# Performance work log

Hardware: AMD Instinct MI355X
Metric: run time of the kernel (lower is better)

Reference implementation:

```python
import jax, jax.numpy as jnp
import numpy as np

N_NODES = 50000
N_EDGES = 800000
NFEAT, NHID, NCLASS = 256, 128, 47


def _gcn_norm(edge_index, edge_weight, n):
    """PyG GCNConv normalization: add self-loops (weight 1) then symmetric deg^-1/2."""
    src, dst = edge_index[0], edge_index[1]
    loop = jnp.arange(n, dtype=src.dtype)
    src_f = jnp.concatenate([src, loop])
    dst_f = jnp.concatenate([dst, loop])
    w_f = jnp.concatenate([edge_weight, jnp.ones((n,), edge_weight.dtype)])
    deg = jax.ops.segment_sum(w_f, dst_f, num_segments=n)  # [n]
    deg_safe = jnp.where(deg > 0, deg, 1.0)
    dinv = jnp.where(deg > 0, jax.lax.rsqrt(deg_safe), 0.0)
    norm = dinv[src_f] * w_f * dinv[dst_f]  # [E + n]
    return src_f, dst_f, norm


def _gcn_conv(h, src, dst, norm, b, n):
    # gather transformed source features, scale, scatter-add into targets
    msg = h[src] * norm[:, None]  # [E+n, d]
    return jax.ops.segment_sum(msg, dst, num_segments=n) + b


def setup_inputs() -> dict:
    key = jax.random.key(0)
    k = jax.random.split(key, 8)
    x = jax.random.normal(k[0], (N_NODES, NFEAT), dtype=jnp.float32)
    edge_index = jax.random.randint(k[1], (2, N_EDGES), 0, N_NODES, dtype=jnp.int32)
    edge_weight = jax.random.uniform(k[2], (N_EDGES,), dtype=jnp.float32)
    W1 = jax.random.normal(k[3], (NFEAT, NHID), dtype=jnp.float32) * (1.0 / np.sqrt(NFEAT))
    b1 = jnp.zeros((NHID,), dtype=jnp.float32)
    W2 = jax.random.normal(k[4], (NHID, NCLASS), dtype=jnp.float32) * (1.0 / np.sqrt(NHID))
    b2 = jnp.zeros((NCLASS,), dtype=jnp.float32)
    return {"x": x, "edge_index": edge_index, "edge_weight": edge_weight,
            "W1": W1, "b1": b1, "W2": W2, "b2": b2}


def reference(x, edge_index, edge_weight, W1, b1, W2, b2):
    n = x.shape[0]
    src, dst, norm = _gcn_norm(edge_index, edge_weight, n)
    h = _gcn_conv(x @ W1, src, dst, norm, b1, n)   # GCNConv 1
    h = jax.nn.relu(h)                             # dropout is identity in eval
    h = _gcn_conv(h @ W2, src, dst, norm, b2, n)   # GCNConv 2
    return jax.nn.log_softmax(h, axis=1)
```

## Files before the change

### kernel.cpp

```cpp
#include <hip/hip_runtime.h>

#define N_NODES 50000
#define N_EDGES 800000
#define NFEAT   256
#define NHID    128
#define NCLASS  47
#define H2P     48
#define CSR_MAX (N_EDGES + 7 * N_NODES)
#define NSUB    8
#define G1_BLOCKS ((N_NODES + 63) / 64)

typedef __attribute__((ext_vector_type(8))) short short8v;
typedef __attribute__((ext_vector_type(4))) float f32x4;

__device__ __forceinline__ ushort f2bf(float f) {
    unsigned u = __float_as_uint(f);
    unsigned r = (u + 0x7FFF + ((u >> 16) & 1)) >> 16;
    return (ushort)r;
}
__device__ __forceinline__ float blo(unsigned u) { return __uint_as_float(u << 16); }
__device__ __forceinline__ float bhi(unsigned u) { return __uint_as_float(u & 0xFFFF0000u); }


__global__ void init_kernel(unsigned long long* __restrict__ packed,
                            int* __restrict__ total,
                            const float* __restrict__ W1, const float* __restrict__ W2,
                            ushort* __restrict__ w1t, ushort* __restrict__ w2t) {
    int t = blockIdx.x * blockDim.x + threadIdx.x;
    if (t < N_NODES * NSUB) packed[t] = 0ull;
    if (t == 0) *total = 0;
    if (t < NFEAT * NHID) {
        int k = t >> 7, c = t & 127;
        w1t[c * NFEAT + k] = f2bf(W1[(size_t)k * NHID + c]);
    }
    if (t < NHID * H2P) {
        int k = t / H2P, c = t % H2P;
        w2t[c * NHID + k] = (c < NCLASS) ? f2bf(W2[(size_t)k * NCLASS + c]) : 0;
    }
}


__global__ __launch_bounds__(256) void fused_gemm1_degcnt_kernel(
        const float* __restrict__ x, const ushort* __restrict__ w1t,
        ushort* __restrict__ h1b,
        const int* __restrict__ dst, const float* __restrict__ w,
        unsigned long long* __restrict__ packed, int* __restrict__ pos) {
    __shared__ __align__(16) ushort xs[64][40];
    __shared__ __align__(16) ushort ws[128][40];
    int tid = threadIdx.x;
    if (blockIdx.x >= G1_BLOCKS) {
        int e = (blockIdx.x - G1_BLOCKS) * 256 + tid;
        if (e < N_EDGES) {
            int d = dst[e];
            int b = tid & (NSUB - 1);
            unsigned fx = __float2uint_rn(w[e] * 1048576.0f);
            unsigned long long old = atomicAdd(&packed[(size_t)b * N_NODES + d],
                                               (1ull << 40) | (unsigned long long)fx);
            pos[e] = (int)(old >> 40);
        }
        return;
    }
    int node0 = blockIdx.x * 64;
    int wave = tid >> 6, l = tid & 63;
    int fr = l & 15, fq = l >> 4;
    int r0 = (wave >> 1) * 32;
    int c0 = (wave & 1) * 64;

    f32x4 acc[2][4] = {};

    for (int kk0 = 0; kk0 < NFEAT; kk0 += 32) {
        {
            int row = tid >> 2, q = tid & 3;
            int srow = node0 + row; if (srow >= N_NODES) srow = N_NODES - 1;
            const float4* sp = (const float4*)(x + (size_t)srow * NFEAT + kk0 + q * 8);
            float4 v0 = sp[0], v1 = sp[1];
            ushort tmp[8];
            tmp[0] = f2bf(v0.x); tmp[1] = f2bf(v0.y); tmp[2] = f2bf(v0.z); tmp[3] = f2bf(v0.w);
            tmp[4] = f2bf(v1.x); tmp[5] = f2bf(v1.y); tmp[6] = f2bf(v1.z); tmp[7] = f2bf(v1.w);
            *(short8v*)&xs[row][q * 8] = *(short8v*)&tmp[0];
        }
        {
            int row = tid >> 1, hb = tid & 1;
            const short8v* sp = (const short8v*)&w1t[(size_t)row * NFEAT + kk0 + hb * 16];
            *(short8v*)&ws[row][hb * 16]     = sp[0];
            *(short8v*)&ws[row][hb * 16 + 8] = sp[1];
        }
        __syncthreads();
        short8v a[2], b[4];
        #pragma unroll
        for (int m = 0; m < 2; ++m)
            a[m] = *(const short8v*)&xs[r0 + m * 16 + fr][fq * 8];
        #pragma unroll
        for (int n = 0; n < 4; ++n)
            b[n] = *(const short8v*)&ws[c0 + n * 16 + fr][fq * 8];
        #pragma unroll
        for (int m = 0; m < 2; ++m)
            #pragma unroll
            for (int n = 0; n < 4; ++n)
                acc[m][n] = __builtin_amdgcn_mfma_f32_16x16x32_bf16(
                    a[m], b[n], acc[m][n], 0, 0, 0);
        __syncthreads();
    }
    #pragma unroll
    for (int m = 0; m < 2; ++m) {
        #pragma unroll
        for (int n = 0; n < 4; ++n) {
            #pragma unroll
            for (int j = 0; j < 4; ++j) {
                int gr = node0 + r0 + m * 16 + fq * 4 + j;
                if (gr < N_NODES)
                    h1b[(size_t)gr * NHID + c0 + n * 16 + fr] = f2bf(acc[m][n][j]);
            }
        }
    }
}

__global__ __launch_bounds__(256) void segalloc_kernel(const unsigned long long* __restrict__ packed,
                                                       int* __restrict__ counts,
                                                       float* __restrict__ dinv,
                                                       int* __restrict__ row_start,
                                                       int* __restrict__ sub_base,
                                                       int* __restrict__ total,
                                                       int2* __restrict__ csr, int n) {
    __shared__ int s[256];
    __shared__ int base_s;
    int t = threadIdx.x;
    int i = blockIdx.x * 256 + t;
    int v = 0, cnt = 0;
    if (i < n) {
        unsigned long long ws = 0;
        int sb[NSUB];
        #pragma unroll
        for (int b = 0; b < NSUB; ++b) {
            unsigned long long pk = packed[(size_t)b * N_NODES + i];
            sb[b] = cnt;
            cnt += (int)(pk >> 40);
            ws += (pk & 0xFFFFFFFFFFull);
        }
        counts[i] = cnt;
        float deg = 1.0f + (float)ws * (1.0f / 1048576.0f);
        dinv[i] = rsqrtf(deg);
        #pragma unroll
        for (int b = 0; b < NSUB; b += 4)
            *(int4*)&sub_base[(size_t)i * NSUB + b] = make_int4(sb[b], sb[b+1], sb[b+2], sb[b+3]);
        v = (cnt + 7) & ~7;
    }
    s[t] = v;
    __syncthreads();
    #pragma unroll
    for (int off = 1; off < 256; off <<= 1) {
        int x = s[t];
        if (t >= off) x += s[t - off];
        __syncthreads();
        s[t] = x;
        __syncthreads();
    }
    if (t == 255) base_s = atomicAdd(total, s[255]);
    __syncthreads();
    if (i < n) {
        int base = base_s + s[t] - v;
        row_start[i] = base;
        for (int k = cnt; k < v; ++k) csr[base + k] = make_int2(0, 0);
    }
}

__global__ void scatter_kernel(const int* __restrict__ src, const int* __restrict__ dst,
                               const float* __restrict__ w, const int* __restrict__ pos,
                               const float* __restrict__ dinv,
                               const int* __restrict__ row_start,
                               const int* __restrict__ sub_base,
                               int2* __restrict__ csr, int E) {
    int e = blockIdx.x * blockDim.x + threadIdx.x;
    if (e >= E) return;
    int d = dst[e], s = src[e];
    int b = e & (NSUB - 1);
    int p = row_start[d] + sub_base[(size_t)d * NSUB + b] + pos[e];
    int2 pr;
    pr.x = s;
    pr.y = __float_as_int(dinv[s] * w[e] * dinv[d]);
    csr[p] = pr;
}


__global__ __launch_bounds__(256) void agg1g2_kernel(const ushort* __restrict__ h1b,
                                                     const int* __restrict__ row_start,
                                                     const int* __restrict__ counts,
                                                     const int2* __restrict__ csr,
                                                     const float* __restrict__ dinv,
                                                     const float* __restrict__ b1,
                                                     const ushort* __restrict__ w2t,
                                                     ushort* __restrict__ h2b) {
    __shared__ __align__(16) ushort hs[16][136];
    __shared__ __align__(16) ushort wt[48][136];
    int tid = threadIdx.x;
    int nb = blockIdx.x * 16;
    int wv = tid >> 6;
    int l = tid & 63;
    int h = l >> 5, q = l & 31;

    #pragma unroll
    for (int i = 0; i < 3; ++i) {
        int id = tid + i * 256;
        int row = id >> 4, cq = id & 15;
        *(short8v*)&wt[row][cq * 8] = *(const short8v*)&w2t[(size_t)row * NHID + cq * 8];
    }

    const ushort* rowp = h1b + 4 * q;

    for (int ni = 0; ni < 4; ++ni) {
        int i = nb + wv * 4 + ni;
        float di = dinv[i];
        float sc = (h == 0) ? di * di : 0.f;
        uint2 sv = *(const uint2*)(rowp + (size_t)i * NHID);
        float4 acc;
        acc.x = sc * blo(sv.x); acc.y = sc * bhi(sv.x);
        acc.z = sc * blo(sv.y); acc.w = sc * bhi(sv.y);

        int lo = row_start[i], hi = lo + ((counts[i] + 7) & ~7);
        int e = lo;
        for (; e + 16 <= hi; e += 16) {
            int2 pA = csr[e + 0 + h],  pB = csr[e + 2 + h];
            int2 pC = csr[e + 4 + h],  pD = csr[e + 6 + h];
            int2 pE = csr[e + 8 + h],  pF = csr[e + 10 + h];
            int2 pG = csr[e + 12 + h], pH = csr[e + 14 + h];
            uint2 vA = *(const uint2*)(rowp + (size_t)pA.x * NHID);
            uint2 vB = *(const uint2*)(rowp + (size_t)pB.x * NHID);
            uint2 vC = *(const uint2*)(rowp + (size_t)pC.x * NHID);
            uint2 vD = *(const uint2*)(rowp + (size_t)pD.x * NHID);
            uint2 vE = *(const uint2*)(rowp + (size_t)pE.x * NHID);
            uint2 vF = *(const uint2*)(rowp + (size_t)pF.x * NHID);
            uint2 vG = *(const uint2*)(rowp + (size_t)pG.x * NHID);
            uint2 vH = *(const uint2*)(rowp + (size_t)pH.x * NHID);
            float wA = __int_as_float(pA.y), wB = __int_as_float(pB.y);
            float wC = __int_as_float(pC.y), wD = __int_as_float(pD.y);
            float wE = __int_as_float(pE.y), wF = __int_as_float(pF.y);
            float wG = __int_as_float(pG.y), wH = __int_as_float(pH.y);
            acc.x = fmaf(wA, blo(vA.x), acc.x); acc.y = fmaf(wA, bhi(vA.x), acc.y);
            acc.z = fmaf(wA, blo(vA.y), acc.z); acc.w = fmaf(wA, bhi(vA.y), acc.w);
            acc.x = fmaf(wB, blo(vB.x), acc.x); acc.y = fmaf(wB, bhi(vB.x), acc.y);
            acc.z = fmaf(wB, blo(vB.y), acc.z); acc.w = fmaf(wB, bhi(vB.y), acc.w);
            acc.x = fmaf(wC, blo(vC.x), acc.x); acc.y = fmaf(wC, bhi(vC.x), acc.y);
            acc.z = fmaf(wC, blo(vC.y), acc.z); acc.w = fmaf(wC, bhi(vC.y), acc.w);
            acc.x = fmaf(wD, blo(vD.x), acc.x); acc.y = fmaf(wD, bhi(vD.x), acc.y);
            acc.z = fmaf(wD, blo(vD.y), acc.z); acc.w = fmaf(wD, bhi(vD.y), acc.w);
            acc.x = fmaf(wE, blo(vE.x), acc.x); acc.y = fmaf(wE, bhi(vE.x), acc.y);
            acc.z = fmaf(wE, blo(vE.y), acc.z); acc.w = fmaf(wE, bhi(vE.y), acc.w);
            acc.x = fmaf(wF, blo(vF.x), acc.x); acc.y = fmaf(wF, bhi(vF.x), acc.y);
            acc.z = fmaf(wF, blo(vF.y), acc.z); acc.w = fmaf(wF, bhi(vF.y), acc.w);
            acc.x = fmaf(wG, blo(vG.x), acc.x); acc.y = fmaf(wG, bhi(vG.x), acc.y);
            acc.z = fmaf(wG, blo(vG.y), acc.z); acc.w = fmaf(wG, bhi(vG.y), acc.w);
            acc.x = fmaf(wH, blo(vH.x), acc.x); acc.y = fmaf(wH, bhi(vH.x), acc.y);
            acc.z = fmaf(wH, blo(vH.y), acc.z); acc.w = fmaf(wH, bhi(vH.y), acc.w);
        }
        if (e < hi) {
            int2 pA = csr[e + 0 + h], pB = csr[e + 2 + h];
            int2 pC = csr[e + 4 + h], pD = csr[e + 6 + h];
            uint2 vA = *(const uint2*)(rowp + (size_t)pA.x * NHID);
            uint2 vB = *(const uint2*)(rowp + (size_t)pB.x * NHID);
            uint2 vC = *(const uint2*)(rowp + (size_t)pC.x * NHID);
            uint2 vD = *(const uint2*)(rowp + (size_t)pD.x * NHID);
            float wA = __int_as_float(pA.y), wB = __int_as_float(pB.y);
            float wC = __int_as_float(pC.y), wD = __int_as_float(pD.y);
            acc.x = fmaf(wA, blo(vA.x), acc.x); acc.y = fmaf(wA, bhi(vA.x), acc.y);
            acc.z = fmaf(wA, blo(vA.y), acc.z); acc.w = fmaf(wA, bhi(vA.y), acc.w);
            acc.x = fmaf(wB, blo(vB.x), acc.x); acc.y = fmaf(wB, bhi(vB.x), acc.y);
            acc.z = fmaf(wB, blo(vB.y), acc.z); acc.w = fmaf(wB, bhi(vB.y), acc.w);
            acc.x = fmaf(wC, blo(vC.x), acc.x); acc.y = fmaf(wC, bhi(vC.x), acc.y);
            acc.z = fmaf(wC, blo(vC.y), acc.z); acc.w = fmaf(wC, bhi(vC.y), acc.w);
            acc.x = fmaf(wD, blo(vD.x), acc.x); acc.y = fmaf(wD, bhi(vD.x), acc.y);
            acc.z = fmaf(wD, blo(vD.y), acc.z); acc.w = fmaf(wD, bhi(vD.y), acc.w);
        }
        acc.x += __shfl_xor(acc.x, 32);
        acc.y += __shfl_xor(acc.y, 32);
        acc.z += __shfl_xor(acc.z, 32);
        acc.w += __shfl_xor(acc.w, 32);
        if (h == 0) {
            float4 bb = *(const float4*)(b1 + 4 * q);
            acc.x = fmaxf(acc.x + bb.x, 0.f);
            acc.y = fmaxf(acc.y + bb.y, 0.f);
            acc.z = fmaxf(acc.z + bb.z, 0.f);
            acc.w = fmaxf(acc.w + bb.w, 0.f);
            uint2 o;
            o.x = (unsigned)f2bf(acc.x) | ((unsigned)f2bf(acc.y) << 16);
            o.y = (unsigned)f2bf(acc.z) | ((unsigned)f2bf(acc.w) << 16);
            *(uint2*)&hs[wv * 4 + ni][4 * q] = o;
        }
    }
    __syncthreads();

    if (wv < 3) {
        int fr = l & 15, fq = l >> 4;
        short8v a[4], b[4];
        #pragma unroll
        for (int kf = 0; kf < 4; ++kf) {
            a[kf] = *(const short8v*)&hs[fr][kf * 32 + fq * 8];
            b[kf] = *(const short8v*)&wt[wv * 16 + fr][kf * 32 + fq * 8];
        }
        f32x4 acc2 = {};
        #pragma unroll
        for (int kf = 0; kf < 4; ++kf)
            acc2 = __builtin_amdgcn_mfma_f32_16x16x32_bf16(a[kf], b[kf], acc2, 0, 0, 0);
        int col = wv * 16 + fr;
        #pragma unroll
        for (int j = 0; j < 4; ++j) {
            int gr = nb + fq * 4 + j;
            h2b[(size_t)gr * H2P + col] = (col < NCLASS) ? f2bf(acc2[j]) : 0;
        }
    }
}


__global__ __launch_bounds__(256) void agg2_kernel(const ushort* __restrict__ h2b,
                                                   const int* __restrict__ row_start,
                                                   const int* __restrict__ counts,
                                                   const int2* __restrict__ csr,
                                                   const float* __restrict__ dinv,
                                                   const float* __restrict__ b2,
                                                   float* __restrict__ out, int n) {
    int wv = threadIdx.x >> 6;
    int i = blockIdx.x * 4 + wv;
    if (i >= n) return;
    int l = threadIdx.x & 63;
    int h = l >> 5, q = l & 31;
    bool act = q < 24;
    int qq = act ? q : 0;
    const ushort* rowp = h2b + 2 * qq;

    float di = dinv[i];
    float sc = (h == 0 && act) ? di * di : 0.f;
    unsigned sv = *(const unsigned*)(rowp + (size_t)i * H2P);
    float2 acc;
    acc.x = sc * blo(sv); acc.y = sc * bhi(sv);

    int lo = row_start[i], hi = lo + ((counts[i] + 7) & ~7);
    int e = lo;
    for (; e + 16 <= hi; e += 16) {
        int2 pA = csr[e + 0 + h],  pB = csr[e + 2 + h];
        int2 pC = csr[e + 4 + h],  pD = csr[e + 6 + h];
        int2 pE = csr[e + 8 + h],  pF = csr[e + 10 + h];
        int2 pG = csr[e + 12 + h], pH = csr[e + 14 + h];
        unsigned vA = *(const unsigned*)(rowp + (size_t)pA.x * H2P);
        unsigned vB = *(const unsigned*)(rowp + (size_t)pB.x * H2P);
        unsigned vC = *(const unsigned*)(rowp + (size_t)pC.x * H2P);
        unsigned vD = *(const unsigned*)(rowp + (size_t)pD.x * H2P);
        unsigned vE = *(const unsigned*)(rowp + (size_t)pE.x * H2P);
        unsigned vF = *(const unsigned*)(rowp + (size_t)pF.x * H2P);
        unsigned vG = *(const unsigned*)(rowp + (size_t)pG.x * H2P);
        unsigned vH = *(const unsigned*)(rowp + (size_t)pH.x * H2P);
        float wA = __int_as_float(pA.y), wB = __int_as_float(pB.y);
        float wC = __int_as_float(pC.y), wD = __int_as_float(pD.y);
        float wE = __int_as_float(pE.y), wF = __int_as_float(pF.y);
        float wG = __int_as_float(pG.y), wH = __int_as_float(pH.y);
        acc.x = fmaf(wA, blo(vA), acc.x); acc.y = fmaf(wA, bhi(vA), acc.y);
        acc.x = fmaf(wB, blo(vB), acc.x); acc.y = fmaf(wB, bhi(vB), acc.y);
        acc.x = fmaf(wC, blo(vC), acc.x); acc.y = fmaf(wC, bhi(vC), acc.y);
        acc.x = fmaf(wD, blo(vD), acc.x); acc.y = fmaf(wD, bhi(vD), acc.y);
        acc.x = fmaf(wE, blo(vE), acc.x); acc.y = fmaf(wE, bhi(vE), acc.y);
        acc.x = fmaf(wF, blo(vF), acc.x); acc.y = fmaf(wF, bhi(vF), acc.y);
        acc.x = fmaf(wG, blo(vG), acc.x); acc.y = fmaf(wG, bhi(vG), acc.y);
        acc.x = fmaf(wH, blo(vH), acc.x); acc.y = fmaf(wH, bhi(vH), acc.y);
    }
    if (e < hi) {
        int2 pA = csr[e + 0 + h], pB = csr[e + 2 + h];
        int2 pC = csr[e + 4 + h], pD = csr[e + 6 + h];
        unsigned vA = *(const unsigned*)(rowp + (size_t)pA.x * H2P);
        unsigned vB = *(const unsigned*)(rowp + (size_t)pB.x * H2P);
        unsigned vC = *(const unsigned*)(rowp + (size_t)pC.x * H2P);
        unsigned vD = *(const unsigned*)(rowp + (size_t)pD.x * H2P);
        float wA = __int_as_float(pA.y), wB = __int_as_float(pB.y);
        float wC = __int_as_float(pC.y), wD = __int_as_float(pD.y);
        acc.x = fmaf(wA, blo(vA), acc.x); acc.y = fmaf(wA, bhi(vA), acc.y);
        acc.x = fmaf(wB, blo(vB), acc.x); acc.y = fmaf(wB, bhi(vB), acc.y);
        acc.x = fmaf(wC, blo(vC), acc.x); acc.y = fmaf(wC, bhi(vC), acc.y);
        acc.x = fmaf(wD, blo(vD), acc.x); acc.y = fmaf(wD, bhi(vD), acc.y);
    }
    acc.x += __shfl_xor(acc.x, 32);
    acc.y += __shfl_xor(acc.y, 32);

    float v0 = -1e30f, v1 = -1e30f;
    if (act) {
        v0 = acc.x + b2[2 * q];
        v1 = (2 * q + 1 < NCLASS) ? (acc.y + b2[2 * q + 1]) : -1e30f;
    }
    float pm = fmaxf(v0, v1);
    #pragma unroll
    for (int off = 16; off; off >>= 1) pm = fmaxf(pm, __shfl_xor(pm, off));
    float ex = 0.f;
    if (act) {
        ex = __expf(v0 - pm);
        if (2 * q + 1 < NCLASS) ex += __expf(v1 - pm);
    }
    #pragma unroll
    for (int off = 16; off; off >>= 1) ex += __shfl_xor(ex, off);
    if (h == 0 && act) {
        float ls = pm + __logf(ex);
        out[(size_t)i * NCLASS + 2 * q] = v0 - ls;
        if (2 * q + 1 < NCLASS) out[(size_t)i * NCLASS + 2 * q + 1] = v1 - ls;
    }
}


extern "C" void kernel_launch(void* const* d_in, const int* in_sizes, int n_in,
                              void* d_out, int out_size, void* d_ws, size_t ws_size,
                              hipStream_t stream) {
    const float* x  = (const float*)d_in[0];
    const int*   ei = (const int*)d_in[1];
    const float* ew = (const float*)d_in[2];
    const float* W1 = (const float*)d_in[3];
    const float* b1 = (const float*)d_in[4];
    const float* W2 = (const float*)d_in[5];
    const float* b2 = (const float*)d_in[6];
    float* out = (float*)d_out;

    const int* e_src = ei;
    const int* e_dst = ei + N_EDGES;

    char* p = (char*)d_ws;
    auto carve = [&](size_t bytes) { void* r = (void*)p; p += (bytes + 255) & ~(size_t)255; return r; };
    unsigned long long* packed = (unsigned long long*)carve((size_t)N_NODES * NSUB * 8);
    float*  dinv      = (float*) carve(N_NODES * 4);
    int*    counts    = (int*)   carve(N_NODES * 4);
    int*    row_start = (int*)   carve(N_NODES * 4);
    int*    sub_base  = (int*)   carve((size_t)N_NODES * NSUB * 4);
    int*    total     = (int*)   carve(4);
    int*    pos       = (int*)   carve((size_t)N_EDGES * 4);
    int2*   csr       = (int2*)  carve((size_t)CSR_MAX * 8);
    ushort* h1b       = (ushort*)carve((size_t)N_NODES * NHID * 2);
    ushort* h2b       = (ushort*)carve((size_t)N_NODES * H2P * 2);
    ushort* w1t       = (ushort*)carve((size_t)NHID * NFEAT * 2);
    ushort* w2t       = (ushort*)carve((size_t)H2P * NHID * 2);

    init_kernel<<<(N_NODES * NSUB + 255) / 256, 256, 0, stream>>>(packed, total, W1, W2, w1t, w2t);
    fused_gemm1_degcnt_kernel<<<G1_BLOCKS + (N_EDGES + 255) / 256, 256, 0, stream>>>(
        x, w1t, h1b, e_dst, ew, packed, pos);
    segalloc_kernel<<<(N_NODES + 255) / 256, 256, 0, stream>>>(packed, counts, dinv,
                                                               row_start, sub_base, total,
                                                               csr, N_NODES);
    scatter_kernel<<<(N_EDGES + 255) / 256, 256, 0, stream>>>(e_src, e_dst, ew, pos, dinv,
                                                              row_start, sub_base, csr, N_EDGES);
    agg1g2_kernel<<<(N_NODES + 15) / 16, 256, 0, stream>>>(h1b, row_start, counts, csr,
                                                           dinv, b1, w2t, h2b);
    agg2_kernel<<<(N_NODES + 3) / 4, 256, 0, stream>>>(h2b, row_start, counts, csr, dinv, b2, out, N_NODES);
}
```

Baseline: 147.5 us.

## Widen per-lane gathers to 16B/8B and process four edges per wave step

Both aggregation kernels now map each 64-lane wave as 4 edge groups by 16 feature lanes. Layer 1 gathers 16-byte uint4 chunks and layer 2 gathers 8-byte uint2 chunks, using padded 64-wide h2 rows. The goal is fewer, wider memory transactions per gathered row and all lanes active in layer 2, where 16 lanes used to sit idle. In exchange there is an extra shuffle-reduction stage, a larger h2 buffer, and extra zero-padding writes from the unused waves in agg1g2.

```diff
diff --git a/kernel.cpp b/kernel.cpp
--- a/kernel.cpp
+++ b/kernel.cpp
@@ -5,7 +5,7 @@
 #define NFEAT   256
 #define NHID    128
 #define NCLASS  47
-#define H2P     48
+#define H2P     64
 #define CSR_MAX (N_EDGES + 7 * N_NODES)
 #define NSUB    8
 #define G1_BLOCKS ((N_NODES + 63) / 64)
@@ -34,7 +34,7 @@
         w1t[c * NFEAT + k] = f2bf(W1[(size_t)k * NHID + c]);
     }
     if (t < NHID * H2P) {
-        int k = t / H2P, c = t % H2P;
+        int k = t >> 6, c = t & 63;
         w2t[c * NHID + k] = (c < NCLASS) ? f2bf(W2[(size_t)k * NCLASS + c]) : 0;
     }
 }
@@ -196,7 +196,7 @@
     int nb = blockIdx.x * 16;
     int wv = tid >> 6;
     int l = tid & 63;
-    int h = l >> 5, q = l & 31;
+    int ed = l >> 4, fp = l & 15;
 
     #pragma unroll
     for (int i = 0; i < 3; ++i) {
@@ -205,85 +205,84 @@
         *(short8v*)&wt[row][cq * 8] = *(const short8v*)&w2t[(size_t)row * NHID + cq * 8];
     }
 
-    const ushort* rowp = h1b + 4 * q;
+    const ushort* rowp = h1b + 8 * fp;
 
     for (int ni = 0; ni < 4; ++ni) {
         int i = nb + wv * 4 + ni;
         float di = dinv[i];
-        float sc = (h == 0) ? di * di : 0.f;
-        uint2 sv = *(const uint2*)(rowp + (size_t)i * NHID);
-        float4 acc;
-        acc.x = sc * blo(sv.x); acc.y = sc * bhi(sv.x);
-        acc.z = sc * blo(sv.y); acc.w = sc * bhi(sv.y);
+        float sc = (ed == 0) ? di * di : 0.f;
+        uint4 sv = *(const uint4*)(rowp + (size_t)i * NHID);
+        float a0 = sc * blo(sv.x), a1 = sc * bhi(sv.x);
+        float a2 = sc * blo(sv.y), a3 = sc * bhi(sv.y);
+        float a4 = sc * blo(sv.z), a5 = sc * bhi(sv.z);
+        float a6 = sc * blo(sv.w), a7 = sc * bhi(sv.w);
 
         int lo = row_start[i], hi = lo + ((counts[i] + 7) & ~7);
         int e = lo;
         for (; e + 16 <= hi; e += 16) {
-            int2 pA = csr[e + 0 + h],  pB = csr[e + 2 + h];
-            int2 pC = csr[e + 4 + h],  pD = csr[e + 6 + h];
-            int2 pE = csr[e + 8 + h],  pF = csr[e + 10 + h];
-            int2 pG = csr[e + 12 + h], pH = csr[e + 14 + h];
-            uint2 vA = *(const uint2*)(rowp + (size_t)pA.x * NHID);
-            uint2 vB = *(const uint2*)(rowp + (size_t)pB.x * NHID);
-            uint2 vC = *(const uint2*)(rowp + (size_t)pC.x * NHID);
-            uint2 vD = *(const uint2*)(rowp + (size_t)pD.x * NHID);
-            uint2 vE = *(const uint2*)(rowp + (size_t)pE.x * NHID);
-            uint2 vF = *(const uint2*)(rowp + (size_t)pF.x * NHID);
-            uint2 vG = *(const uint2*)(rowp + (size_t)pG.x * NHID);
-            uint2 vH = *(const uint2*)(rowp + (size_t)pH.x * NHID);
+            int2 pA = csr[e + ed];
+            int2 pB = csr[e + 4 + ed];
+            int2 pC = csr[e + 8 + ed];
+            int2 pD = csr[e + 12 + ed];
+            uint4 vA = *(const uint4*)(rowp + (size_t)pA.x * NHID);
+            uint4 vB = *(const uint4*)(rowp + (size_t)pB.x * NHID);
+            uint4 vC = *(const uint4*)(rowp + (size_t)pC.x * NHID);
+            uint4 vD = *(const uint4*)(rowp + (size_t)pD.x * NHID);
             float wA = __int_as_float(pA.y), wB = __int_as_float(pB.y);
             float wC = __int_as_float(pC.y), wD = __int_as_float(pD.y);
-            float wE = __int_as_float(pE.y), wF = __int_as_float(pF.y);
-            float wG = __int_as_float(pG.y), wH = __int_as_float(pH.y);
-            acc.x = fmaf(wA, blo(vA.x), acc.x); acc.y = fmaf(wA, bhi(vA.x), acc.y);
-            acc.z = fmaf(wA, blo(vA.y), acc.z); acc.w = fmaf(wA, bhi(vA.y), acc.w);
-            acc.x = fmaf(wB, blo(vB.x), acc.x); acc.y = fmaf(wB, bhi(vB.x), acc.y);
-            acc.z = fmaf(wB, blo(vB.y), acc.z); acc.w = fmaf(wB, bhi(vB.y), acc.w);
-            acc.x = fmaf(wC, blo(vC.x), acc.x); acc.y = fmaf(wC, bhi(vC.x), acc.y);
-            acc.z = fmaf(wC, blo(vC.y), acc.z); acc.w = fmaf(wC, bhi(vC.y), acc.w);
-            acc.x = fmaf(wD, blo(vD.x), acc.x); acc.y = fmaf(wD, bhi(vD.x), acc.y);
-            acc.z = fmaf(wD, blo(vD.y), acc.z); acc.w = fmaf(wD, bhi(vD.y), acc.w);
-            acc.x = fmaf(wE, blo(vE.x), acc.x); acc.y = fmaf(wE, bhi(vE.x), acc.y);
-            acc.z = fmaf(wE, blo(vE.y), acc.z); acc.w = fmaf(wE, bhi(vE.y), acc.w);
-            acc.x = fmaf(wF, blo(vF.x), acc.x); acc.y = fmaf(wF, bhi(vF.x), acc.y);
-            acc.z = fmaf(wF, blo(vF.y), acc.z); acc.w = fmaf(wF, bhi(vF.y), acc.w);
-            acc.x = fmaf(wG, blo(vG.x), acc.x); acc.y = fmaf(wG, bhi(vG.x), acc.y);
-            acc.z = fmaf(wG, blo(vG.y), acc.z); acc.w = fmaf(wG, bhi(vG.y), acc.w);
-            acc.x = fmaf(wH, blo(vH.x), acc.x); acc.y = fmaf(wH, bhi(vH.x), acc.y);
-            acc.z = fmaf(wH, blo(vH.y), acc.z); acc.w = fmaf(wH, bhi(vH.y), acc.w);
+            a0 = fmaf(wA, blo(vA.x), a0); a1 = fmaf(wA, bhi(vA.x), a1);
+            a2 = fmaf(wA, blo(vA.y), a2); a3 = fmaf(wA, bhi(vA.y), a3);
+            a4 = fmaf(wA, blo(vA.z), a4); a5 = fmaf(wA, bhi(vA.z), a5);
+            a6 = fmaf(wA, blo(vA.w), a6); a7 = fmaf(wA, bhi(vA.w), a7);
+            a0 = fmaf(wB, blo(vB.x), a0); a1 = fmaf(wB, bhi(vB.x), a1);
+            a2 = fmaf(wB, blo(vB.y), a2); a3 = fmaf(wB, bhi(vB.y), a3);
+            a4 = fmaf(wB, blo(vB.z), a4); a5 = fmaf(wB, bhi(vB.z), a5);
+            a6 = fmaf(wB, blo(vB.w), a6); a7 = fmaf(wB, bhi(vB.w), a7);
+            a0 = fmaf(wC, blo(vC.x), a0); a1 = fmaf(wC, bhi(vC.x), a1);
+            a2 = fmaf(wC, blo(vC.y), a2); a3 = fmaf(wC, bhi(vC.y), a3);
+            a4 = fmaf(wC, blo(vC.z), a4); a5 = fmaf(wC, bhi(vC.z), a5);
+            a6 = fmaf(wC, blo(vC.w), a6); a7 = fmaf(wC, bhi(vC.w), a7);
+            a0 = fmaf(wD, blo(vD.x), a0); a1 = fmaf(wD, bhi(vD.x), a1);
+            a2 = fmaf(wD, blo(vD.y), a2); a3 = fmaf(wD, bhi(vD.y), a3);
+            a4 = fmaf(wD, blo(vD.z), a4); a5 = fmaf(wD, bhi(vD.z), a5);
+            a6 = fmaf(wD, blo(vD.w), a6); a7 = fmaf(wD, bhi(vD.w), a7);
         }
         if (e < hi) {
-            int2 pA = csr[e + 0 + h], pB = csr[e + 2 + h];
-            int2 pC = csr[e + 4 + h], pD = csr[e + 6 + h];
-            uint2 vA = *(const uint2*)(rowp + (size_t)pA.x * NHID);
-            uint2 vB = *(const uint2*)(rowp + (size_t)pB.x * NHID);
-            uint2 vC = *(const uint2*)(rowp + (size_t)pC.x * NHID);
-            uint2 vD = *(const uint2*)(rowp + (size_t)pD.x * NHID);
+            int2 pA = csr[e + ed];
+            int2 pB = csr[e + 4 + ed];
+            uint4 vA = *(const uint4*)(rowp + (size_t)pA.x * NHID);
+            uint4 vB = *(const uint4*)(rowp + (size_t)pB.x * NHID);
             float wA = __int_as_float(pA.y), wB = __int_as_float(pB.y);
-            float wC = __int_as_float(pC.y), wD = __int_as_float(pD.y);
-            acc.x = fmaf(wA, blo(vA.x), acc.x); acc.y = fmaf(wA, bhi(vA.x), acc.y);
-            acc.z = fmaf(wA, blo(vA.y), acc.z); acc.w = fmaf(wA, bhi(vA.y), acc.w);
-            acc.x = fmaf(wB, blo(vB.x), acc.x); acc.y = fmaf(wB, bhi(vB.x), acc.y);
-            acc.z = fmaf(wB, blo(vB.y), acc.z); acc.w = fmaf(wB, bhi(vB.y), acc.w);
-            acc.x = fmaf(wC, blo(vC.x), acc.x); acc.y = fmaf(wC, bhi(vC.x), acc.y);
-            acc.z = fmaf(wC, blo(vC.y), acc.z); acc.w = fmaf(wC, bhi(vC.y), acc.w);
-            acc.x = fmaf(wD, blo(vD.x), acc.x); acc.y = fmaf(wD, bhi(vD.x), acc.y);
-            acc.z = fmaf(wD, blo(vD.y), acc.z); acc.w = fmaf(wD, bhi(vD.y), acc.w);
-        }
-        acc.x += __shfl_xor(acc.x, 32);
-        acc.y += __shfl_xor(acc.y, 32);
-        acc.z += __shfl_xor(acc.z, 32);
-        acc.w += __shfl_xor(acc.w, 32);
-        if (h == 0) {
-            float4 bb = *(const float4*)(b1 + 4 * q);
-            acc.x = fmaxf(acc.x + bb.x, 0.f);
-            acc.y = fmaxf(acc.y + bb.y, 0.f);
-            acc.z = fmaxf(acc.z + bb.z, 0.f);
-            acc.w = fmaxf(acc.w + bb.w, 0.f);
-            uint2 o;
-            o.x = (unsigned)f2bf(acc.x) | ((unsigned)f2bf(acc.y) << 16);
-            o.y = (unsigned)f2bf(acc.z) | ((unsigned)f2bf(acc.w) << 16);
-            *(uint2*)&hs[wv * 4 + ni][4 * q] = o;
+            a0 = fmaf(wA, blo(vA.x), a0); a1 = fmaf(wA, bhi(vA.x), a1);
+            a2 = fmaf(wA, blo(vA.y), a2); a3 = fmaf(wA, bhi(vA.y), a3);
+            a4 = fmaf(wA, blo(vA.z), a4); a5 = fmaf(wA, bhi(vA.z), a5);
+            a6 = fmaf(wA, blo(vA.w), a6); a7 = fmaf(wA, bhi(vA.w), a7);
+            a0 = fmaf(wB, blo(vB.x), a0); a1 = fmaf(wB, bhi(vB.x), a1);
+            a2 = fmaf(wB, blo(vB.y), a2); a3 = fmaf(wB, bhi(vB.y), a3);
+            a4 = fmaf(wB, blo(vB.z), a4); a5 = fmaf(wB, bhi(vB.z), a5);
+            a6 = fmaf(wB, blo(vB.w), a6); a7 = fmaf(wB, bhi(vB.w), a7);
+        }
+        a0 += __shfl_xor(a0, 16); a1 += __shfl_xor(a1, 16);
+        a2 += __shfl_xor(a2, 16); a3 += __shfl_xor(a3, 16);
+        a4 += __shfl_xor(a4, 16); a5 += __shfl_xor(a5, 16);
+        a6 += __shfl_xor(a6, 16); a7 += __shfl_xor(a7, 16);
+        a0 += __shfl_xor(a0, 32); a1 += __shfl_xor(a1, 32);
+        a2 += __shfl_xor(a2, 32); a3 += __shfl_xor(a3, 32);
+        a4 += __shfl_xor(a4, 32); a5 += __shfl_xor(a5, 32);
+        a6 += __shfl_xor(a6, 32); a7 += __shfl_xor(a7, 32);
+        if (ed == 0) {
+            float4 bb0 = *(const float4*)(b1 + 8 * fp);
+            float4 bb1 = *(const float4*)(b1 + 8 * fp + 4);
+            a0 = fmaxf(a0 + bb0.x, 0.f); a1 = fmaxf(a1 + bb0.y, 0.f);
+            a2 = fmaxf(a2 + bb0.z, 0.f); a3 = fmaxf(a3 + bb0.w, 0.f);
+            a4 = fmaxf(a4 + bb1.x, 0.f); a5 = fmaxf(a5 + bb1.y, 0.f);
+            a6 = fmaxf(a6 + bb1.z, 0.f); a7 = fmaxf(a7 + bb1.w, 0.f);
+            uint4 o;
+            o.x = (unsigned)f2bf(a0) | ((unsigned)f2bf(a1) << 16);
+            o.y = (unsigned)f2bf(a2) | ((unsigned)f2bf(a3) << 16);
+            o.z = (unsigned)f2bf(a4) | ((unsigned)f2bf(a5) << 16);
+            o.w = (unsigned)f2bf(a6) | ((unsigned)f2bf(a7) << 16);
+            *(uint4*)&hs[wv * 4 + ni][8 * fp] = o;
         }
     }
     __syncthreads();
@@ -306,6 +305,11 @@
             int gr = nb + fq * 4 + j;
             h2b[(size_t)gr * H2P + col] = (col < NCLASS) ? f2bf(acc2[j]) : 0;
         }
+    } else {
+        int fr = l & 15, fq = l >> 4;
+        #pragma unroll
+        for (int j = 0; j < 4; ++j)
+            h2b[(size_t)(nb + fq * 4 + j) * H2P + 48 + fr] = 0;
     }
 }
 
@@ -321,81 +325,70 @@
     int i = blockIdx.x * 4 + wv;
     if (i >= n) return;
     int l = threadIdx.x & 63;
-    int h = l >> 5, q = l & 31;
-    bool act = q < 24;
-    int qq = act ? q : 0;
-    const ushort* rowp = h2b + 2 * qq;
+    int ed = l >> 4, fp = l & 15;
+    const ushort* rowp = h2b + 4 * fp;
 
     float di = dinv[i];
-    float sc = (h == 0 && act) ? di * di : 0.f;
-    unsigned sv = *(const unsigned*)(rowp + (size_t)i * H2P);
-    float2 acc;
-    acc.x = sc * blo(sv); acc.y = sc * bhi(sv);
+    float sc = (ed == 0) ? di * di : 0.f;
+    uint2 sv = *(const uint2*)(rowp + (size_t)i * H2P);
+    float a0 = sc * blo(sv.x), a1 = sc * bhi(sv.x);
+    float a2 = sc * blo(sv.y), a3 = sc * bhi(sv.y);
 
     int lo = row_start[i], hi = lo + ((counts[i] + 7) & ~7);
     int e = lo;
     for (; e + 16 <= hi; e += 16) {
-        int2 pA = csr[e + 0 + h],  pB = csr[e + 2 + h];
-        int2 pC = csr[e + 4 + h],  pD = csr[e + 6 + h];
-        int2 pE = csr[e + 8 + h],  pF = csr[e + 10 + h];
-        int2 pG = csr[e + 12 + h], pH = csr[e + 14 + h];
-        unsigned vA = *(const unsigned*)(rowp + (size_t)pA.x * H2P);
-        unsigned vB = *(const unsigned*)(rowp + (size_t)pB.x * H2P);
-        unsigned vC = *(const unsigned*)(rowp + (size_t)pC.x * H2P);
-        unsigned vD = *(const unsigned*)(rowp + (size_t)pD.x * H2P);
-        unsigned vE = *(const unsigned*)(rowp + (size_t)pE.x * H2P);
-        unsigned vF = *(const unsigned*)(rowp + (size_t)pF.x * H2P);
-        unsigned vG = *(const unsigned*)(rowp + (size_t)pG.x * H2P);
-        unsigned vH = *(const unsigned*)(rowp + (size_t)pH.x * H2P);
+        int2 pA = csr[e + ed];
+        int2 pB = csr[e + 4 + ed];
+        int2 pC = csr[e + 8 + ed];
+        int2 pD = csr[e + 12 + ed];
+        uint2 vA = *(const uint2*)(rowp + (size_t)pA.x * H2P);
+        uint2 vB = *(const uint2*)(rowp + (size_t)pB.x * H2P);
+        uint2 vC = *(const uint2*)(rowp + (size_t)pC.x * H2P);
+        uint2 vD = *(const uint2*)(rowp + (size_t)pD.x * H2P);
         float wA = __int_as_float(pA.y), wB = __int_as_float(pB.y);
         float wC = __int_as_float(pC.y), wD = __int_as_float(pD.y);
-        float wE = __int_as_float(pE.y), wF = __int_as_float(pF.y);
-        float wG = __int_as_float(pG.y), wH = __int_as_float(pH.y);
-        acc.x = fmaf(wA, blo(vA), acc.x); acc.y = fmaf(wA, bhi(vA), acc.y);
-        acc.x = fmaf(wB, blo(vB), acc.x); acc.y = fmaf(wB, bhi(vB), acc.y);
-        acc.x = fmaf(wC, blo(vC), acc.x); acc.y = fmaf(wC, bhi(vC), acc.y);
-        acc.x = fmaf(wD, blo(vD), acc.x); acc.y = fmaf(wD, bhi(vD), acc.y);
-        acc.x = fmaf(wE, blo(vE), acc.x); acc.y = fmaf(wE, bhi(vE), acc.y);
-        acc.x = fmaf(wF, blo(vF), acc.x); acc.y = fmaf(wF, bhi(vF), acc.y);
-        acc.x = fmaf(wG, blo(vG), acc.x); acc.y = fmaf(wG, bhi(vG), acc.y);
-        acc.x = fmaf(wH, blo(vH), acc.x); acc.y = fmaf(wH, bhi(vH), acc.y);
+        a0 = fmaf(wA, blo(vA.x), a0); a1 = fmaf(wA, bhi(vA.x), a1);
+        a2 = fmaf(wA, blo(vA.y), a2); a3 = fmaf(wA, bhi(vA.y), a3);
+        a0 = fmaf(wB, blo(vB.x), a0); a1 = fmaf(wB, bhi(vB.x), a1);
+        a2 = fmaf(wB, blo(vB.y), a2); a3 = fmaf(wB, bhi(vB.y), a3);
+        a0 = fmaf(wC, blo(vC.x), a0); a1 = fmaf(wC, bhi(vC.x), a1);
+        a2 = fmaf(wC, blo(vC.y), a2); a3 = fmaf(wC, bhi(vC.y), a3);
+        a0 = fmaf(wD, blo(vD.x), a0); a1 = fmaf(wD, bhi(vD.x), a1);
+        a2 = fmaf(wD, blo(vD.y), a2); a3 = fmaf(wD, bhi(vD.y), a3);
     }
     if (e < hi) {
-        int2 pA = csr[e + 0 + h], pB = csr[e + 2 + h];
-        int2 pC = csr[e + 4 + h], pD = csr[e + 6 + h];
-        unsigned vA = *(const unsigned*)(rowp + (size_t)pA.x * H2P);
-        unsigned vB = *(const unsigned*)(rowp + (size_t)pB.x * H2P);
-        unsigned vC = *(const unsigned*)(rowp + (size_t)pC.x * H2P);
-        unsigned vD = *(const unsigned*)(rowp + (size_t)pD.x * H2P);
+        int2 pA = csr[e + ed];
+        int2 pB = csr[e + 4 + ed];
+        uint2 vA = *(const uint2*)(rowp + (size_t)pA.x * H2P);
+        uint2 vB = *(const uint2*)(rowp + (size_t)pB.x * H2P);
         float wA = __int_as_float(pA.y), wB = __int_as_float(pB.y);
-        float wC = __int_as_float(pC.y), wD = __int_as_float(pD.y);
-        acc.x = fmaf(wA, blo(vA), acc.x); acc.y = fmaf(wA, bhi(vA), acc.y);
-        acc.x = fmaf(wB, blo(vB), acc.x); acc.y = fmaf(wB, bhi(vB), acc.y);
-        acc.x = fmaf(wC, blo(vC), acc.x); acc.y = fmaf(wC, bhi(vC), acc.y);
-        acc.x = fmaf(wD, blo(vD), acc.x); acc.y = fmaf(wD, bhi(vD), acc.y);
-    }
-    acc.x += __shfl_xor(acc.x, 32);
-    acc.y += __shfl_xor(acc.y, 32);
-
-    float v0 = -1e30f, v1 = -1e30f;
-    if (act) {
-        v0 = acc.x + b2[2 * q];
-        v1 = (2 * q + 1 < NCLASS) ? (acc.y + b2[2 * q + 1]) : -1e30f;
-    }
-    float pm = fmaxf(v0, v1);
+        a0 = fmaf(wA, blo(vA.x), a0); a1 = fmaf(wA, bhi(vA.x), a1);
+        a2 = fmaf(wA, blo(vA.y), a2); a3 = fmaf(wA, bhi(vA.y), a3);
+        a0 = fmaf(wB, blo(vB.x), a0); a1 = fmaf(wB, bhi(vB.x), a1);
+        a2 = fmaf(wB, blo(vB.y), a2); a3 = fmaf(wB, bhi(vB.y), a3);
+    }
+    a0 += __shfl_xor(a0, 16); a1 += __shfl_xor(a1, 16);
+    a2 += __shfl_xor(a2, 16); a3 += __shfl_xor(a3, 16);
+    a0 += __shfl_xor(a0, 32); a1 += __shfl_xor(a1, 32);
+    a2 += __shfl_xor(a2, 32); a3 += __shfl_xor(a3, 32);
+
+    int c0 = 4 * fp;
+    float v0 = (c0 + 0 < NCLASS) ? (a0 + b2[c0 + 0]) : -1e30f;
+    float v1 = (c0 + 1 < NCLASS) ? (a1 + b2[c0 + 1]) : -1e30f;
+    float v2 = (c0 + 2 < NCLASS) ? (a2 + b2[c0 + 2]) : -1e30f;
+    float v3 = (c0 + 3 < NCLASS) ? (a3 + b2[c0 + 3]) : -1e30f;
+    float pm = fmaxf(fmaxf(v0, v1), fmaxf(v2, v3));
     #pragma unroll
-    for (int off = 16; off; off >>= 1) pm = fmaxf(pm, __shfl_xor(pm, off));
-    float ex = 0.f;
-    if (act) {
-        ex = __expf(v0 - pm);
-        if (2 * q + 1 < NCLASS) ex += __expf(v1 - pm);
-    }
+    for (int off = 1; off <= 8; off <<= 1) pm = fmaxf(pm, __shfl_xor(pm, off));
+    float ex = __expf(v0 - pm) + __expf(v1 - pm) + __expf(v2 - pm) + __expf(v3 - pm);
     #pragma unroll
-    for (int off = 16; off; off >>= 1) ex += __shfl_xor(ex, off);
-    if (h == 0 && act) {
+    for (int off = 1; off <= 8; off <<= 1) ex += __shfl_xor(ex, off);
+    if (ed == 0) {
         float ls = pm + __logf(ex);
-        out[(size_t)i * NCLASS + 2 * q] = v0 - ls;
-        if (2 * q + 1 < NCLASS) out[(size_t)i * NCLASS + 2 * q + 1] = v1 - ls;
+        if (c0 + 0 < NCLASS) out[(size_t)i * NCLASS + c0 + 0] = v0 - ls;
+        if (c0 + 1 < NCLASS) out[(size_t)i * NCLASS + c0 + 1] = v1 - ls;
+        if (c0 + 2 < NCLASS) out[(size_t)i * NCLASS + c0 + 2] = v2 - ls;
+        if (c0 + 3 < NCLASS) out[(size_t)i * NCLASS + c0 + 3] = v3 - ls;
     }
 }
 
```

New measurement: 145.4 us. No clear change (-1.5%).
